# Kernel tuning notes

Hardware: AMD Instinct MI355X
Metric: run time of the kernel (lower is better)

Reference implementation:

```python
import jax, jax.numpy as jnp
import numpy as np

HIDDEN = 64


def _lstm_cell(x, h, c, W_ih, W_hh, b_ih, b_hh):
    # gates: [B, 4*H], torch LSTMCell order: i, f, g, o
    gates = x @ W_ih.T + h @ W_hh.T + b_ih + b_hh
    i, f, g, o = jnp.split(gates, 4, axis=-1)
    i = jax.nn.sigmoid(i)
    f = jax.nn.sigmoid(f)
    g = jnp.tanh(g)
    o = jax.nn.sigmoid(o)
    c_new = f * c + i * g
    h_new = o * jnp.tanh(c_new)
    return h_new, c_new


def setup_inputs() -> dict:
    key = jax.random.key(0)
    ks = jax.random.split(key, 12)
    B, L, H = 1024, 512, HIDDEN
    k = 1.0 / np.sqrt(H)  # torch LSTMCell/Linear init scale
    u = lambda kk, shape: jax.random.uniform(kk, shape, jnp.float32, -k, k)
    return {
        "y": jax.random.normal(ks[0], (B, L), jnp.float32),
        "W_ih1": u(ks[1], (4 * H, 1)),
        "W_hh1": u(ks[2], (4 * H, H)),
        "b_ih1": u(ks[3], (4 * H,)),
        "b_hh1": u(ks[4], (4 * H,)),
        "W_ih2": u(ks[5], (4 * H, H)),
        "W_hh2": u(ks[6], (4 * H, H)),
        "b_ih2": u(ks[7], (4 * H,)),
        "b_hh2": u(ks[8], (4 * H,)),
        "W_lin": u(ks[9], (1, H)),
        "b_lin": u(ks[10], (1,)),
        "future_preds": 0,
    }


def reference(y, W_ih1, W_hh1, b_ih1, b_hh1, W_ih2, W_hh2, b_ih2, b_hh2,
              W_lin, b_lin, future_preds):
    B = y.shape[0]
    H = HIDDEN
    zeros = jnp.zeros((B, H), jnp.float32)

    def step(carry, x_t):
        h1, c1, h2, c2 = carry
        h1, c1 = _lstm_cell(x_t, h1, c1, W_ih1, W_hh1, b_ih1, b_hh1)
        h2, c2 = _lstm_cell(h1, h2, c2, W_ih2, W_hh2, b_ih2, b_hh2)
        out = h2 @ W_lin.T + b_lin  # [B, 1]
        return (h1, c1, h2, c2), out

    xs = y.T[:, :, None]  # [L, B, 1]
    carry, outs = jax.lax.scan(step, (zeros, zeros, zeros, zeros), xs)
    outputs = outs[:, :, 0].T  # [B, L]

    if future_preds > 0:
        def fstep(fc, _):
            h1, c1, h2, c2, out = fc
            h1, c1 = _lstm_cell(out, h1, c1, W_ih1, W_hh1, b_ih1, b_hh1)
            h2, c2 = _lstm_cell(h1, h2, c2, W_ih2, W_hh2, b_ih2, b_hh2)
            out = h2 @ W_lin.T + b_lin
            return (h1, c1, h2, c2, out), out
        last_out = outs[-1]  # [B, 1]
        _, fouts = jax.lax.scan(fstep, (*carry, last_out), None,
                                length=future_preds)
        outputs = jnp.concatenate([outputs, fouts[:, :, 0].T], axis=1)
    return outputs
```

## Files before the change

kernel.cpp:

```cpp
#include <hip/hip_runtime.h>
#include <math.h>

#define LSEQ 512

typedef float  f32x4  __attribute__((ext_vector_type(4)));
typedef short  bf16x8 __attribute__((ext_vector_type(8)));

union Frag { uint32_t u[4]; bf16x8 h; };

__device__ __forceinline__ float frcp(float x) { return __builtin_amdgcn_rcpf(x); }

__device__ __forceinline__ f32x4 vexp2(f32x4 x) {
    f32x4 r;
    r.x = exp2f(x.x); r.y = exp2f(x.y); r.z = exp2f(x.z); r.w = exp2f(x.w);
    return r;
}
__device__ __forceinline__ f32x4 vrcp(f32x4 x) {
    f32x4 r;
    r.x = frcp(x.x); r.y = frcp(x.y); r.z = frcp(x.z); r.w = frcp(x.w);
    return r;
}
__device__ __forceinline__ f32x4 vsigm(f32x4 x) {
    f32x4 e = vexp2(x * -1.442695041f);
    return vrcp(e + 1.0f);
}
__device__ __forceinline__ f32x4 vtanh(f32x4 x) {
    f32x4 e = vexp2(x * 2.885390082f);
    return 1.0f - 2.0f * vrcp(e + 1.0f);
}

__device__ __forceinline__ uint32_t pack_hi_u(uint32_t b0, uint32_t b1) {
    return __builtin_amdgcn_perm(b1, b0, 0x07060302u);
}

__device__ __forceinline__ void load_wfrag(const float* __restrict__ W, int sl, int nn, int g4,
                                           Frag fh[4][2], Frag fl[4][2]) {
#pragma unroll
    for (int gt = 0; gt < 4; ++gt) {
        const float* p = W + (size_t)(64 * gt + 16 * sl + nn) * 64 + g4 * 8;
#pragma unroll
        for (int kt = 0; kt < 2; ++kt) {
            float4 va = ((const float4*)(p + kt * 32))[0];
            float4 vb = ((const float4*)(p + kt * 32))[1];
            float v[8] = {va.x, va.y, va.z, va.w, vb.x, vb.y, vb.z, vb.w};
#pragma unroll
            for (int j = 0; j < 4; ++j) {
                uint32_t b0 = __float_as_uint(v[2 * j]);
                uint32_t b1 = __float_as_uint(v[2 * j + 1]);
                float l0 = v[2 * j]     - __uint_as_float(b0 & 0xffff0000u);
                float l1 = v[2 * j + 1] - __uint_as_float(b1 & 0xffff0000u);
                fh[gt][kt].u[j] = pack_hi_u(b0, b1);
                fl[gt][kt].u[j] = pack_hi_u(__float_as_uint(l0), __float_as_uint(l1));
            }
        }
    }
}

__device__ __forceinline__ int hidx(int m, int j) {
    return m * 64 + ((((j >> 3) ^ (m & 7)) << 3) | (j & 7));
}

__device__ __forceinline__ void loadA(const uint16_t* __restrict__ ph,
                                      const uint16_t* __restrict__ pl,
                                      int mm, int g4, bf16x8 ah[2], bf16x8 al[2]) {
#pragma unroll
    for (int kt = 0; kt < 2; ++kt) {
        const int off = mm * 64 + ((((kt << 2) + g4) ^ (mm & 7)) << 3);
        ah[kt] = *(const bf16x8*)(ph + off);
        al[kt] = *(const bf16x8*)(pl + off);
    }
}

__device__ __forceinline__ void split_store(uint16_t* ph, uint16_t* pl, int idx, float x) {
    uint32_t xb = __float_as_uint(x);
    ph[idx] = (uint16_t)(xb >> 16);
    float lo = x - __uint_as_float(xb & 0xffff0000u);
    pl[idx] = (uint16_t)(__float_as_uint(lo) >> 16);
}

#define MFMA3(acc, AH, AL, BH, BL)                                                  \
    acc = __builtin_amdgcn_mfma_f32_16x16x32_bf16((AH), (BH).h, acc, 0, 0, 0);      \
    acc = __builtin_amdgcn_mfma_f32_16x16x32_bf16((AH), (BL).h, acc, 0, 0, 0);      \
    acc = __builtin_amdgcn_mfma_f32_16x16x32_bf16((AL), (BH).h, acc, 0, 0, 0);

__global__ __launch_bounds__(512, 1)
void lstm2_pipe(const float* __restrict__ y,
                const float* __restrict__ W_ih1, const float* __restrict__ W_hh1,
                const float* __restrict__ b_ih1, const float* __restrict__ b_hh1,
                const float* __restrict__ W_ih2, const float* __restrict__ W_hh2,
                const float* __restrict__ b_ih2, const float* __restrict__ b_hh2,
                const float* __restrict__ W_lin, const float* __restrict__ b_lin,
                float* __restrict__ out)
{
    __shared__ __align__(16) float    y_s[LSEQ * 16];
    __shared__ __align__(16) uint16_t h1h[2][1024];
    __shared__ __align__(16) uint16_t h1l[2][1024];
    __shared__ __align__(16) uint16_t h2h[2][1024];
    __shared__ __align__(16) uint16_t h2l[2][1024];
    __shared__ __align__(16) float    outS[LSEQ * 20];

    const int tid  = threadIdx.x;
    const int w    = tid >> 6;
    const int lane = tid & 63;
    const int nn   = lane & 15;
    const int g4   = lane >> 4;
    const int mq   = g4 << 2;
    const int bg0  = blockIdx.x << 4;

    {
        const int m = tid >> 5, seg = tid & 31;
        const float4* yp = (const float4*)(y + (size_t)(bg0 + m) * LSEQ) + seg * 4;
#pragma unroll
        for (int c = 0; c < 4; ++c) {
            float4 v = yp[c];
            int t0 = seg * 16 + c * 4;
            y_s[(t0 + 0) * 16 + m] = v.x;
            y_s[(t0 + 1) * 16 + m] = v.y;
            y_s[(t0 + 2) * 16 + m] = v.z;
            y_s[(t0 + 3) * 16 + m] = v.w;
        }
        if (tid < 256) {
            uint4 z = {0u, 0u, 0u, 0u};
            ((uint4*)h1h)[tid] = z;
            ((uint4*)h1l)[tid] = z;
            ((uint4*)h2h)[tid] = z;
            ((uint4*)h2l)[tid] = z;
        }
    }
    __syncthreads();

    if (w < 4) {
        Frag bh[4][2], bl[4][2];
        load_wfrag(W_hh1, w, nn, g4, bh, bl);
        float bs1_[4], wih1_[4];
#pragma unroll
        for (int gt = 0; gt < 4; ++gt) {
            int row = 64 * gt + 16 * w + nn;
            bs1_[gt]  = b_ih1[row] + b_hh1[row];
            wih1_[gt] = W_ih1[row];
        }
        const int jj = 16 * w + nn;
        f32x4 c1v = {0.f, 0.f, 0.f, 0.f};
        const float blin = b_lin[0];

        Frag wlh[2], wll[2];
#pragma unroll
        for (int kt = 0; kt < 2; ++kt) {
            if (nn == 0) {
                const float* p = W_lin + kt * 32 + g4 * 8;
                float4 va = ((const float4*)p)[0];
                float4 vb = ((const float4*)p)[1];
                float vv[8] = {va.x, va.y, va.z, va.w, vb.x, vb.y, vb.z, vb.w};
#pragma unroll
                for (int j = 0; j < 4; ++j) {
                    uint32_t b0 = __float_as_uint(vv[2 * j]);
                    uint32_t b1 = __float_as_uint(vv[2 * j + 1]);
                    float l0 = vv[2 * j]     - __uint_as_float(b0 & 0xffff0000u);
                    float l1 = vv[2 * j + 1] - __uint_as_float(b1 & 0xffff0000u);
                    wlh[kt].u[j] = pack_hi_u(b0, b1);
                    wll[kt].u[j] = pack_hi_u(__float_as_uint(l0), __float_as_uint(l1));
                }
            } else {
                wlh[kt].u[0] = wlh[kt].u[1] = wlh[kt].u[2] = wlh[kt].u[3] = 0u;
                wll[kt].u[0] = wll[kt].u[1] = wll[kt].u[2] = wll[kt].u[3] = 0u;
            }
        }

#pragma unroll 1
        for (int t = 0; t <= LSEQ + 1; ++t) {
            if (t < LSEQ) {
                bf16x8 ah[2], al[2];
                loadA(h1h[(t + 1) & 1], h1l[(t + 1) & 1], nn, g4, ah, al);
                f32x4 xq = *(const f32x4*)&y_s[t * 16 + mq];
                f32x4 ac0[4], ac1[4];
#pragma unroll
                for (int g = 0; g < 4; ++g) {
                    ac0[g] = xq * wih1_[g] + bs1_[g];
                    ac1[g] = 0.f;
                }
                __builtin_amdgcn_s_setprio(1);
#pragma unroll
                for (int g = 0; g < 4; ++g) {
                    MFMA3(ac0[g], ah[0], al[0], bh[g][0], bl[g][0]);
                    MFMA3(ac1[g], ah[1], al[1], bh[g][1], bl[g][1]);
                }
                __builtin_amdgcn_s_setprio(0);
                f32x4 gi = vsigm(ac0[0] + ac1[0]);
                f32x4 gf = vsigm(ac0[1] + ac1[1]);
                f32x4 gg = vtanh(ac0[2] + ac1[2]);
                f32x4 go = vsigm(ac0[3] + ac1[3]);
                c1v = gf * c1v + gi * gg;
                f32x4 h1v = go * vtanh(c1v);
#pragma unroll
                for (int r = 0; r < 4; ++r)
                    split_store(h1h[t & 1], h1l[t & 1], hidx(mq + r, jj), h1v[r]);
            }
            if (w == 3 && t >= 3) {
                bf16x8 a3h_[2], a3l_[2];
                loadA(h2h[(t + 1) & 1], h2l[(t + 1) & 1], nn, g4, a3h_, a3l_);
                f32x4 accD = {0.f, 0.f, 0.f, 0.f};
                MFMA3(accD, a3h_[0], a3l_[0], wlh[0], wll[0]);
                MFMA3(accD, a3h_[1], a3l_[1], wlh[1], wll[1]);
                if (nn == 0) {
                    *(f32x4*)&outS[(t - 3) * 20 + mq] = accD + blin;
                }
            }
            __syncthreads();
        }
        if (w == 3) {
            bf16x8 a3h_[2], a3l_[2];
            loadA(h2h[1], h2l[1], nn, g4, a3h_, a3l_);
            f32x4 accD = {0.f, 0.f, 0.f, 0.f};
            MFMA3(accD, a3h_[0], a3l_[0], wlh[0], wll[0]);
            MFMA3(accD, a3h_[1], a3l_[1], wlh[1], wll[1]);
            if (nn == 0) {
                *(f32x4*)&outS[(LSEQ - 1) * 20 + mq] = accD + blin;
            }
        }
    } else {
        const int v = w - 4;
        Frag bih[4][2], bil[4][2], bhh[4][2], bhl[4][2];
        load_wfrag(W_ih2, v, nn, g4, bih, bil);
        load_wfrag(W_hh2, v, nn, g4, bhh, bhl);
        float bs2_[4];
#pragma unroll
        for (int gt = 0; gt < 4; ++gt) {
            int row = 64 * gt + 16 * v + nn;
            bs2_[gt] = b_ih2[row] + b_hh2[row];
        }
        const int jj = 16 * v + nn;
        f32x4 c2v = {0.f, 0.f, 0.f, 0.f};
        f32x4 ihA[4];
#pragma unroll
        for (int g = 0; g < 4; ++g) ihA[g] = 0.f;

#pragma unroll 1
        for (int t = 0; t <= LSEQ + 1; ++t) {
            if (t >= 2) {
                bf16x8 a3h_[2], a3l_[2];
                loadA(h2h[(t + 1) & 1], h2l[(t + 1) & 1], nn, g4, a3h_, a3l_);
                f32x4 acb0[4], acb1[4];
#pragma unroll
                for (int g = 0; g < 4; ++g) { acb0[g] = 0.f; acb1[g] = 0.f; }
                __builtin_amdgcn_s_setprio(1);
#pragma unroll
                for (int g = 0; g < 4; ++g) {
                    MFMA3(acb0[g], a3h_[0], a3l_[0], bhh[g][0], bhl[g][0]);
                    MFMA3(acb1[g], a3h_[1], a3l_[1], bhh[g][1], bhl[g][1]);
                }
                __builtin_amdgcn_s_setprio(0);
                f32x4 gi = vsigm(ihA[0] + acb0[0] + acb1[0]);
                f32x4 gf = vsigm(ihA[1] + acb0[1] + acb1[1]);
                f32x4 gg = vtanh(ihA[2] + acb0[2] + acb1[2]);
                f32x4 go = vsigm(ihA[3] + acb0[3] + acb1[3]);
                c2v = gf * c2v + gi * gg;
                f32x4 h2v = go * vtanh(c2v);
#pragma unroll
                for (int r = 0; r < 4; ++r)
                    split_store(h2h[t & 1], h2l[t & 1], hidx(mq + r, jj), h2v[r]);
            }
            if (t >= 1 && t <= LSEQ) {
                bf16x8 a2h_[2], a2l_[2];
                loadA(h1h[(t + 1) & 1], h1l[(t + 1) & 1], nn, g4, a2h_, a2l_);
                f32x4 aca0[4], aca1[4];
#pragma unroll
                for (int g = 0; g < 4; ++g) { aca0[g] = bs2_[g]; aca1[g] = 0.f; }
#pragma unroll
                for (int g = 0; g < 4; ++g) {
                    MFMA3(aca0[g], a2h_[0], a2l_[0], bih[g][0], bil[g][0]);
                    MFMA3(aca1[g], a2h_[1], a2l_[1], bih[g][1], bil[g][1]);
                }
#pragma unroll
                for (int g = 0; g < 4; ++g) ihA[g] = aca0[g] + aca1[g];
            }
            __syncthreads();
        }
    }

    __syncthreads();

    {
        const int m  = tid >> 5;
        const int t0 = (tid & 31) << 4;
        float* op = out + (size_t)(bg0 + m) * LSEQ + t0;
#pragma unroll
        for (int k2 = 0; k2 < 4; ++k2) {
            float4 vv = make_float4(outS[(t0 + 4 * k2 + 0) * 20 + m],
                                    outS[(t0 + 4 * k2 + 1) * 20 + m],
                                    outS[(t0 + 4 * k2 + 2) * 20 + m],
                                    outS[(t0 + 4 * k2 + 3) * 20 + m]);
            *(float4*)(op + 4 * k2) = vv;
        }
    }
}

extern "C" void kernel_launch(void* const* d_in, const int* in_sizes, int n_in,
                              void* d_out, int out_size, void* d_ws, size_t ws_size,
                              hipStream_t stream) {
    const float* y     = (const float*)d_in[0];
    const float* W_ih1 = (const float*)d_in[1];
    const float* W_hh1 = (const float*)d_in[2];
    const float* b_ih1 = (const float*)d_in[3];
    const float* b_hh1 = (const float*)d_in[4];
    const float* W_ih2 = (const float*)d_in[5];
    const float* W_hh2 = (const float*)d_in[6];
    const float* b_ih2 = (const float*)d_in[7];
    const float* b_hh2 = (const float*)d_in[8];
    const float* W_lin = (const float*)d_in[9];
    const float* b_lin = (const float*)d_in[10];
    float* out = (float*)d_out;

    lstm2_pipe<<<dim3(64), dim3(512), 0, stream>>>(
        y, W_ih1, W_hh1, b_ih1, b_hh1, W_ih2, W_hh2, b_ih2, b_hh2,
        W_lin, b_lin, out);
}
```

Measured before the change: 837.8 us.

## Split each LSTM layer across eight waves with paired-gate MFMA tiles

Doubles the block to 1024 threads so each layer uses 8 waves instead of 4. Each wave now computes 8 hidden units with two gates packed per 16-column MFMA tile, halving per-wave MFMA and activation work on the serial recurrence. The activation is restructured so lanes 0-7 compute tanh/sigmoid and lanes 8-15 sigmoid, and a lane shuffle exchanges the i*g products. This trades shorter per-step critical paths for more waves per barrier, extra shuffles, and half the lanes idling on stores.

```diff
diff --git a/kernel.cpp b/kernel.cpp
--- a/kernel.cpp
+++ b/kernel.cpp
@@ -10,38 +10,21 @@
 
 __device__ __forceinline__ float frcp(float x) { return __builtin_amdgcn_rcpf(x); }
 
-__device__ __forceinline__ f32x4 vexp2(f32x4 x) {
-    f32x4 r;
-    r.x = exp2f(x.x); r.y = exp2f(x.y); r.z = exp2f(x.z); r.w = exp2f(x.w);
-    return r;
-}
-__device__ __forceinline__ f32x4 vrcp(f32x4 x) {
-    f32x4 r;
-    r.x = frcp(x.x); r.y = frcp(x.y); r.z = frcp(x.z); r.w = frcp(x.w);
-    return r;
-}
-__device__ __forceinline__ f32x4 vsigm(f32x4 x) {
-    f32x4 e = vexp2(x * -1.442695041f);
-    return vrcp(e + 1.0f);
-}
-__device__ __forceinline__ f32x4 vtanh(f32x4 x) {
-    f32x4 e = vexp2(x * 2.885390082f);
-    return 1.0f - 2.0f * vrcp(e + 1.0f);
-}
-
 __device__ __forceinline__ uint32_t pack_hi_u(uint32_t b0, uint32_t b1) {
     return __builtin_amdgcn_perm(b1, b0, 0x07060302u);
 }
 
-__device__ __forceinline__ void load_wfrag(const float* __restrict__ W, int sl, int nn, int g4,
-                                           Frag fh[4][2], Frag fl[4][2]) {
-#pragma unroll
-    for (int gt = 0; gt < 4; ++gt) {
-        const float* p = W + (size_t)(64 * gt + 16 * sl + nn) * 64 + g4 * 8;
+__device__ __forceinline__ void load_wfrag8(const float* __restrict__ W, int sl, int nn, int g4,
+                                            Frag fh[2][2], Frag fl[2][2]) {
+#pragma unroll
+    for (int p = 0; p < 2; ++p) {
+        const int gate = 2 * p + (nn >> 3);
+        const int row  = 64 * gate + 8 * sl + (nn & 7);
+        const float* ptr = W + (size_t)row * 64 + g4 * 8;
 #pragma unroll
         for (int kt = 0; kt < 2; ++kt) {
-            float4 va = ((const float4*)(p + kt * 32))[0];
-            float4 vb = ((const float4*)(p + kt * 32))[1];
+            float4 va = ((const float4*)(ptr + kt * 32))[0];
+            float4 vb = ((const float4*)(ptr + kt * 32))[1];
             float v[8] = {va.x, va.y, va.z, va.w, vb.x, vb.y, vb.z, vb.w};
 #pragma unroll
             for (int j = 0; j < 4; ++j) {
@@ -49,8 +32,8 @@
                 uint32_t b1 = __float_as_uint(v[2 * j + 1]);
                 float l0 = v[2 * j]     - __uint_as_float(b0 & 0xffff0000u);
                 float l1 = v[2 * j + 1] - __uint_as_float(b1 & 0xffff0000u);
-                fh[gt][kt].u[j] = pack_hi_u(b0, b1);
-                fl[gt][kt].u[j] = pack_hi_u(__float_as_uint(l0), __float_as_uint(l1));
+                fh[p][kt].u[j] = pack_hi_u(b0, b1);
+                fl[p][kt].u[j] = pack_hi_u(__float_as_uint(l0), __float_as_uint(l1));
             }
         }
     }
@@ -83,7 +66,36 @@
     acc = __builtin_amdgcn_mfma_f32_16x16x32_bf16((AH), (BL).h, acc, 0, 0, 0);      \
     acc = __builtin_amdgcn_mfma_f32_16x16x32_bf16((AL), (BH).h, acc, 0, 0, 0);
 
-__global__ __launch_bounds__(512, 1)
+__device__ __forceinline__ f32x4 act2t(f32x4 a0, f32x4 a1, f32x4& c,
+                                       float kk1, float aa1, float bb1) {
+    f32x4 s0, s1, th;
+#pragma unroll
+    for (int r = 0; r < 4; ++r) s0[r] = frcp(1.0f + exp2f(-1.442695041f * a0[r]));
+#pragma unroll
+    for (int r = 0; r < 4; ++r) s1[r] = fmaf(bb1, frcp(exp2f(kk1 * a1[r]) + 1.0f), aa1);
+    f32x4 ig = s0 * s1;
+    f32x4 igx;
+#pragma unroll
+    for (int r = 0; r < 4; ++r) igx[r] = __shfl_xor(ig[r], 8, 64);
+    c = s0 * c + igx;
+#pragma unroll
+    for (int r = 0; r < 4; ++r) {
+        float e = exp2f(2.885390082f * c[r]);
+        th[r] = fmaf(-2.0f, frcp(e + 1.0f), 1.0f);
+    }
+    return s1 * th;
+}
+
+__device__ __forceinline__ void store_h8(uint16_t* ph, uint16_t* pl, int sl, int nn, int mq,
+                                         f32x4 hv) {
+    if (nn >= 8) {
+        const int j = 8 * sl + (nn & 7);
+#pragma unroll
+        for (int r = 0; r < 4; ++r) split_store(ph, pl, hidx(mq + r, j), hv[r]);
+    }
+}
+
+__global__ __launch_bounds__(1024, 1)
 void lstm2_pipe(const float* __restrict__ y,
                 const float* __restrict__ W_ih1, const float* __restrict__ W_hh1,
                 const float* __restrict__ b_ih1, const float* __restrict__ b_hh1,
@@ -107,13 +119,17 @@
     const int mq   = g4 << 2;
     const int bg0  = blockIdx.x << 4;
 
+    const float kk1 = (nn < 8) ? 2.885390082f : -1.442695041f;
+    const float aa1 = (nn < 8) ? 1.0f : 0.0f;
+    const float bb1 = (nn < 8) ? -2.0f : 1.0f;
+
     {
-        const int m = tid >> 5, seg = tid & 31;
-        const float4* yp = (const float4*)(y + (size_t)(bg0 + m) * LSEQ) + seg * 4;
-#pragma unroll
-        for (int c = 0; c < 4; ++c) {
+        const int m = tid >> 6, seg = tid & 63;
+        const float4* yp = (const float4*)(y + (size_t)(bg0 + m) * LSEQ + seg * 8);
+#pragma unroll
+        for (int c = 0; c < 2; ++c) {
             float4 v = yp[c];
-            int t0 = seg * 16 + c * 4;
+            int t0 = seg * 8 + c * 4;
             y_s[(t0 + 0) * 16 + m] = v.x;
             y_s[(t0 + 1) * 16 + m] = v.y;
             y_s[(t0 + 2) * 16 + m] = v.z;
@@ -129,24 +145,23 @@
     }
     __syncthreads();
 
-    if (w < 4) {
-        Frag bh[4][2], bl[4][2];
-        load_wfrag(W_hh1, w, nn, g4, bh, bl);
-        float bs1_[4], wih1_[4];
-#pragma unroll
-        for (int gt = 0; gt < 4; ++gt) {
-            int row = 64 * gt + 16 * w + nn;
-            bs1_[gt]  = b_ih1[row] + b_hh1[row];
-            wih1_[gt] = W_ih1[row];
-        }
-        const int jj = 16 * w + nn;
+    if (w < 8) {
+        Frag bh[2][2], bl[2][2];
+        load_wfrag8(W_hh1, w, nn, g4, bh, bl);
+        float bs1_[2], wih1_[2];
+#pragma unroll
+        for (int p = 0; p < 2; ++p) {
+            const int row = 64 * (2 * p + (nn >> 3)) + 8 * w + (nn & 7);
+            bs1_[p]  = b_ih1[row] + b_hh1[row];
+            wih1_[p] = W_ih1[row];
+        }
         f32x4 c1v = {0.f, 0.f, 0.f, 0.f};
         const float blin = b_lin[0];
 
         Frag wlh[2], wll[2];
 #pragma unroll
         for (int kt = 0; kt < 2; ++kt) {
-            if (nn == 0) {
+            if (w == 7 && nn == 0) {
                 const float* p = W_lin + kt * 32 + g4 * 8;
                 float4 va = ((const float4*)p)[0];
                 float4 vb = ((const float4*)p)[1];
@@ -172,30 +187,23 @@
                 bf16x8 ah[2], al[2];
                 loadA(h1h[(t + 1) & 1], h1l[(t + 1) & 1], nn, g4, ah, al);
                 f32x4 xq = *(const f32x4*)&y_s[t * 16 + mq];
-                f32x4 ac0[4], ac1[4];
-#pragma unroll
-                for (int g = 0; g < 4; ++g) {
-                    ac0[g] = xq * wih1_[g] + bs1_[g];
-                    ac1[g] = 0.f;
+                f32x4 ac0[2], ac1[2];
+#pragma unroll
+                for (int p = 0; p < 2; ++p) {
+                    ac0[p] = xq * wih1_[p] + bs1_[p];
+                    ac1[p] = 0.f;
                 }
                 __builtin_amdgcn_s_setprio(1);
 #pragma unroll
-                for (int g = 0; g < 4; ++g) {
-                    MFMA3(ac0[g], ah[0], al[0], bh[g][0], bl[g][0]);
-                    MFMA3(ac1[g], ah[1], al[1], bh[g][1], bl[g][1]);
+                for (int p = 0; p < 2; ++p) {
+                    MFMA3(ac0[p], ah[0], al[0], bh[p][0], bl[p][0]);
+                    MFMA3(ac1[p], ah[1], al[1], bh[p][1], bl[p][1]);
                 }
                 __builtin_amdgcn_s_setprio(0);
-                f32x4 gi = vsigm(ac0[0] + ac1[0]);
-                f32x4 gf = vsigm(ac0[1] + ac1[1]);
-                f32x4 gg = vtanh(ac0[2] + ac1[2]);
-                f32x4 go = vsigm(ac0[3] + ac1[3]);
-                c1v = gf * c1v + gi * gg;
-                f32x4 h1v = go * vtanh(c1v);
-#pragma unroll
-                for (int r = 0; r < 4; ++r)
-                    split_store(h1h[t & 1], h1l[t & 1], hidx(mq + r, jj), h1v[r]);
-            }
-            if (w == 3 && t >= 3) {
+                f32x4 hv = act2t(ac0[0] + ac1[0], ac0[1] + ac1[1], c1v, kk1, aa1, bb1);
+                store_h8(h1h[t & 1], h1l[t & 1], w, nn, mq, hv);
+            }
+            if (w == 7 && t >= 3) {
                 bf16x8 a3h_[2], a3l_[2];
                 loadA(h2h[(t + 1) & 1], h2l[(t + 1) & 1], nn, g4, a3h_, a3l_);
                 f32x4 accD = {0.f, 0.f, 0.f, 0.f};
@@ -207,7 +215,7 @@
             }
             __syncthreads();
         }
-        if (w == 3) {
+        if (w == 7) {
             bf16x8 a3h_[2], a3l_[2];
             loadA(h2h[1], h2l[1], nn, g4, a3h_, a3l_);
             f32x4 accD = {0.f, 0.f, 0.f, 0.f};
@@ -218,60 +226,48 @@
             }
         }
     } else {
-        const int v = w - 4;
-        Frag bih[4][2], bil[4][2], bhh[4][2], bhl[4][2];
-        load_wfrag(W_ih2, v, nn, g4, bih, bil);
-        load_wfrag(W_hh2, v, nn, g4, bhh, bhl);
-        float bs2_[4];
-#pragma unroll
-        for (int gt = 0; gt < 4; ++gt) {
-            int row = 64 * gt + 16 * v + nn;
-            bs2_[gt] = b_ih2[row] + b_hh2[row];
-        }
-        const int jj = 16 * v + nn;
+        const int v = w - 8;
+        Frag bih[2][2], bil[2][2], bhh[2][2], bhl[2][2];
+        load_wfrag8(W_ih2, v, nn, g4, bih, bil);
+        load_wfrag8(W_hh2, v, nn, g4, bhh, bhl);
+        float bs2_[2];
+#pragma unroll
+        for (int p = 0; p < 2; ++p) {
+            const int row = 64 * (2 * p + (nn >> 3)) + 8 * v + (nn & 7);
+            bs2_[p] = b_ih2[row] + b_hh2[row];
+        }
         f32x4 c2v = {0.f, 0.f, 0.f, 0.f};
-        f32x4 ihA[4];
-#pragma unroll
-        for (int g = 0; g < 4; ++g) ihA[g] = 0.f;
+        f32x4 ihA[2];
+        ihA[0] = 0.f; ihA[1] = 0.f;
 
 #pragma unroll 1
         for (int t = 0; t <= LSEQ + 1; ++t) {
             if (t >= 2) {
                 bf16x8 a3h_[2], a3l_[2];
                 loadA(h2h[(t + 1) & 1], h2l[(t + 1) & 1], nn, g4, a3h_, a3l_);
-                f32x4 acb0[4], acb1[4];
-#pragma unroll
-                for (int g = 0; g < 4; ++g) { acb0[g] = 0.f; acb1[g] = 0.f; }
+                f32x4 ac[2];
+                ac[0] = ihA[0]; ac[1] = ihA[1];
                 __builtin_amdgcn_s_setprio(1);
 #pragma unroll
-                for (int g = 0; g < 4; ++g) {
-                    MFMA3(acb0[g], a3h_[0], a3l_[0], bhh[g][0], bhl[g][0]);
-                    MFMA3(acb1[g], a3h_[1], a3l_[1], bhh[g][1], bhl[g][1]);
+                for (int p = 0; p < 2; ++p) {
+                    MFMA3(ac[p], a3h_[0], a3l_[0], bhh[p][0], bhl[p][0]);
+                    MFMA3(ac[p], a3h_[1], a3l_[1], bhh[p][1], bhl[p][1]);
                 }
                 __builtin_amdgcn_s_setprio(0);
-                f32x4 gi = vsigm(ihA[0] + acb0[0] + acb1[0]);
-                f32x4 gf = vsigm(ihA[1] + acb0[1] + acb1[1]);
-                f32x4 gg = vtanh(ihA[2] + acb0[2] + acb1[2]);
-                f32x4 go = vsigm(ihA[3] + acb0[3] + acb1[3]);
-                c2v = gf * c2v + gi * gg;
-                f32x4 h2v = go * vtanh(c2v);
-#pragma unroll
-                for (int r = 0; r < 4; ++r)
-                    split_store(h2h[t & 1], h2l[t & 1], hidx(mq + r, jj), h2v[r]);
+                f32x4 hv = act2t(ac[0], ac[1], c2v, kk1, aa1, bb1);
+                store_h8(h2h[t & 1], h2l[t & 1], v, nn, mq, hv);
             }
             if (t >= 1 && t <= LSEQ) {
                 bf16x8 a2h_[2], a2l_[2];
                 loadA(h1h[(t + 1) & 1], h1l[(t + 1) & 1], nn, g4, a2h_, a2l_);
-                f32x4 aca0[4], aca1[4];
-#pragma unroll
-                for (int g = 0; g < 4; ++g) { aca0[g] = bs2_[g]; aca1[g] = 0.f; }
-#pragma unroll
-                for (int g = 0; g < 4; ++g) {
-                    MFMA3(aca0[g], a2h_[0], a2l_[0], bih[g][0], bil[g][0]);
-                    MFMA3(aca1[g], a2h_[1], a2l_[1], bih[g][1], bil[g][1]);
-                }
-#pragma unroll
-                for (int g = 0; g < 4; ++g) ihA[g] = aca0[g] + aca1[g];
+                f32x4 ai[2];
+                ai[0] = bs2_[0]; ai[1] = bs2_[1];
+#pragma unroll
+                for (int p = 0; p < 2; ++p) {
+                    MFMA3(ai[p], a2h_[0], a2l_[0], bih[p][0], bil[p][0]);
+                    MFMA3(ai[p], a2h_[1], a2l_[1], bih[p][1], bil[p][1]);
+                }
+                ihA[0] = ai[0]; ihA[1] = ai[1];
             }
             __syncthreads();
         }
@@ -280,11 +276,11 @@
     __syncthreads();
 
     {
-        const int m  = tid >> 5;
-        const int t0 = (tid & 31) << 4;
+        const int m  = tid >> 6;
+        const int t0 = (tid & 63) << 3;
         float* op = out + (size_t)(bg0 + m) * LSEQ + t0;
 #pragma unroll
-        for (int k2 = 0; k2 < 4; ++k2) {
+        for (int k2 = 0; k2 < 2; ++k2) {
             float4 vv = make_float4(outS[(t0 + 4 * k2 + 0) * 20 + m],
                                     outS[(t0 + 4 * k2 + 1) * 20 + m],
                                     outS[(t0 + 4 * k2 + 2) * 20 + m],
@@ -310,7 +306,7 @@
     const float* b_lin = (const float*)d_in[10];
     float* out = (float*)d_out;
 
-    lstm2_pipe<<<dim3(64), dim3(512), 0, stream>>>(
+    lstm2_pipe<<<dim3(64), dim3(1024), 0, stream>>>(
         y, W_ih1, W_hh1, b_ih1, b_hh1, W_ih2, W_hh2, b_ih2, b_hh2,
         W_lin, b_lin, out);
 }
```

After: 924.5 us. +10.3%, slower.
